# Performance work log

Measured on AMD Instinct MI355X. Metric: run time of the kernel, lower is better.

The kernel has to match this reference:

```python
import jax, jax.numpy as jnp
import numpy as np

B, S, D = 4, 2048, 1024
H, DK, DV = 16, 64, 64  # heads, key_size, size_per_head
NEG = 1000000000.0


def setup_inputs() -> dict:
    key = jax.random.key(0)
    ks = jax.random.split(key, 8)
    scale = 1.0 / np.sqrt(D)
    return {
        "q": jax.random.normal(ks[0], (B, S, D), jnp.float32),
        "k": jax.random.normal(ks[1], (B, S, D), jnp.float32),
        "v": jax.random.normal(ks[2], (B, S, D), jnp.float32),
        "v_mask": jax.random.randint(ks[3], (B, S), 0, 2).astype(jnp.float32),
        "q_mask": jax.random.randint(ks[4], (B, S), 0, 2).astype(jnp.float32),
        "Wq": jax.random.normal(ks[5], (D, H * DK), jnp.float32) * scale,
        "Wk": jax.random.normal(ks[6], (D, H * DK), jnp.float32) * scale,
        "Wv": jax.random.normal(ks[7], (D, H * DV), jnp.float32) * scale,
    }


def reference(q, k, v, v_mask, q_mask, Wq, Wk, Wv):
    b, sq, _ = q.shape
    sk = k.shape[1]
    # projections + head split: [B, H, S, Dh]
    qw = (q @ Wq).reshape(b, sq, H, DK).transpose(0, 2, 1, 3)
    kw = (k @ Wk).reshape(b, sk, H, DK).transpose(0, 2, 1, 3)
    vw = (v @ Wv).reshape(b, sk, H, DV).transpose(0, 2, 1, 3)
    # scaled dot-product scores [B, H, Sq, Sk]
    a = jnp.einsum("bhqd,bhkd->bhqk", qw, kw) / jnp.sqrt(jnp.float32(DK))
    # additive kv-mask (v_mask over key axis)
    a = a - (1.0 - v_mask)[:, None, None, :] * NEG
    # causal (mask_right=True): subtract 1e9 on strictly-upper triangle
    causal = jnp.triu(jnp.ones((sq, sk), jnp.float32), k=1) * NEG
    a = a - causal[None, None]
    a = jax.nn.softmax(a, axis=-1)
    o = jnp.einsum("bhqk,bhkd->bhqd", a, vw)
    o = o.transpose(0, 2, 1, 3).reshape(b, sq, H * DV)
    # multiplicative query mask on output
    return o * q_mask[:, :, None]
```

## Files before the change

kernel.cpp:

```cpp
#include <hip/hip_runtime.h>

#define S_LEN 2048
#define NHEAD 16

typedef float f32x4 __attribute__((ext_vector_type(4)));
typedef __bf16 bf16x8 __attribute__((ext_vector_type(8)));
typedef __bf16 bf16x4 __attribute__((ext_vector_type(4)));

#define AS1 __attribute__((address_space(1)))
#define AS3 __attribute__((address_space(3)))

__device__ __forceinline__ void gl2lds16(const void* g, void* l) {
    __builtin_amdgcn_global_load_lds((const AS1 unsigned int*)g,
                                     (AS3 unsigned int*)l, 16, 0, 0);
}
__device__ __forceinline__ void wb_leave4() {
    asm volatile("s_waitcnt vmcnt(4)\n\ts_barrier" ::: "memory");
}
__device__ __forceinline__ void wb_drain() {
    asm volatile("s_waitcnt vmcnt(0)\n\ts_barrier" ::: "memory");
}

__global__ __launch_bounds__(256) void cast_swizzle_kernel(
    const float* __restrict__ q, const float* __restrict__ k,
    const float* __restrict__ v, __bf16* __restrict__ out)
{
    int gid = blockIdx.x * 256 + threadIdx.x;
    int z   = gid >> 20;
    int rem = gid & 1048575;
    int r   = rem >> 7;
    int c   = rem & 127;
    const float* src = (z == 0 ? q : z == 1 ? k : v) + (size_t)r * 1024 + c * 8;
    float4 a = *(const float4*)src;
    float4 b = *(const float4*)(src + 4);
    bf16x8 t;
    t[0] = (__bf16)a.x; t[1] = (__bf16)a.y; t[2] = (__bf16)a.z; t[3] = (__bf16)a.w;
    t[4] = (__bf16)b.x; t[5] = (__bf16)b.y; t[6] = (__bf16)b.z; t[7] = (__bf16)b.w;
    int cp = (c & ~7) | ((c ^ r) & 7);
    *(bf16x8*)(out + (size_t)z * 8388608 + (size_t)r * 1024 + cp * 8) = t;
}

__global__ __launch_bounds__(256) void transpose_cast_kernel(
    const float* __restrict__ W0, const float* __restrict__ W1,
    const float* __restrict__ W2, __bf16* __restrict__ Wt)
{
    int z = blockIdx.z;
    const float* W = (z == 0 ? W0 : z == 1 ? W1 : W2);
    __bf16* out = Wt + (size_t)z * 1048576;
    __shared__ float tile[32][33];
    int bx = blockIdx.x, by = blockIdx.y;
    int tid = threadIdx.x;
    int tx = tid & 31, ty = tid >> 5;
    for (int i = 0; i < 32; i += 8)
        tile[ty + i][tx] = W[(size_t)(by * 32 + ty + i) * 1024 + bx * 32 + tx];
    __syncthreads();
    if (tid < 128) {
        int nl = tid >> 2, kc = tid & 3;
        int n = bx * 32 + nl;
        int kbase = by * 32 + kc * 8;
        bf16x8 t;
        for (int j = 0; j < 8; j++) t[j] = (__bf16)tile[kc * 8 + j][nl];
        int cp = ((kbase >> 3) ^ n) & 7;
        *(bf16x8*)(out + (size_t)n * 1024 + (kbase & ~63) + cp * 8) = t;
    }
}

__global__ __launch_bounds__(256, 3) void proj_gemm_kernel(
    const __bf16* __restrict__ Abf, const __bf16* __restrict__ Wt,
    __bf16* __restrict__ qw, __bf16* __restrict__ kw, __bf16* __restrict__ vt)
{
    int z = blockIdx.z;
    const __bf16* A = Abf + (size_t)z * 8388608;
    const __bf16* B = Wt + (size_t)z * 1048576;
    __shared__ __align__(16) char smem[49152];

    int tid = threadIdx.x;
    int bm = blockIdx.x, bn = blockIdx.y;
    int wave = tid >> 6, lane = tid & 63;
    int wm = (wave >> 1) * 64, wn = (wave & 1) * 64;
    int lrow = lane & 15;
    int q4 = lane >> 4;
    int l4r = lane >> 2, j4 = lane & 3;

    auto pf = [&](int kb) {
        int sl = kb % 3;
        int k0 = kb * 32;
        int segbyte = (k0 >> 6) * 128;
        int cbase = (k0 & 32) >> 3;
        for (int i = 0; i < 2; i++) {
            int r = wave * 32 + i * 16 + l4r;
            int cl = j4 ^ ((r >> 1) & 3);
            int phys = ((cbase + cl) ^ r) & 7;
            gl2lds16((const char*)A + (size_t)(bm * 128 + r) * 2048 + segbyte + phys * 16,
                     smem + sl * 8192 + wave * 2048 + i * 1024);
            gl2lds16((const char*)B + (size_t)(bn * 128 + r) * 2048 + segbyte + phys * 16,
                     smem + 24576 + sl * 8192 + wave * 2048 + i * 1024);
        }
    };

    f32x4 zero = {0.f, 0.f, 0.f, 0.f};
    f32x4 acc[4][4];
    for (int mt = 0; mt < 4; mt++)
        for (int nt = 0; nt < 4; nt++) acc[mt][nt] = zero;

    pf(0); pf(1);
    __syncthreads();
    for (int kb = 0; kb < 32; kb++) {
        if (kb == 31) wb_drain(); else wb_leave4();
        if (kb + 2 < 32) pf(kb + 2);
        int sA = (kb % 3) * 8192, sB = 24576 + (kb % 3) * 8192;
        bf16x8 af[4], bfv[4];
        for (int mt = 0; mt < 4; mt++) {
            int r = wm + mt * 16 + lrow;
            af[mt] = *(const bf16x8*)(smem + sA + r * 64 + (q4 ^ ((r >> 1) & 3)) * 16);
        }
        for (int nt = 0; nt < 4; nt++) {
            int r = wn + nt * 16 + lrow;
            bfv[nt] = *(const bf16x8*)(smem + sB + r * 64 + (q4 ^ ((r >> 1) & 3)) * 16);
        }
        for (int mt = 0; mt < 4; mt++)
            for (int nt = 0; nt < 4; nt++)
                acc[mt][nt] = __builtin_amdgcn_mfma_f32_16x16x32_bf16(
                    af[mt], bfv[nt], acc[mt][nt], 0, 0, 0);
    }
    __syncthreads();
    __bf16* T = (__bf16*)smem;

    float oscale = (z == 0) ? 0.125f : 1.0f;
    int rowoff = q4 * 4;
    int b = bm >> 4;
    int s_base = (bm & 15) * 128;
    if (z < 2) {
        for (int mt = 0; mt < 4; mt++) {
            for (int nt = 0; nt < 4; nt++) {
                int n_local = wn + nt * 16 + lrow;
                int hl = n_local >> 6, d = n_local & 63;
                for (int reg = 0; reg < 4; reg++) {
                    int s_local = wm + mt * 16 + rowoff + reg;
                    int s = s_base + s_local;
                    int dp = (d & 7) | ((((d >> 3) ^ s) & 7) << 3);
                    T[s_local * 136 + hl * 64 + dp] = (__bf16)(acc[mt][nt][reg] * oscale);
                }
            }
        }
        __syncthreads();
        char* gq = (char*)(z == 0 ? qw : kw);
        for (int i = 0; i < 8; i++) {
            int id = tid + i * 256;
            int hl = id >> 10, r = (id >> 3) & 127, j = id & 7;
            float4 val = *(float4*)((char*)T + r * 272 + hl * 128 + j * 16);
            *(float4*)(gq + ((size_t)((b * 16 + bn * 2 + hl) * 2048) + s_base + r) * 128
                          + j * 16) = val;
        }
    } else {
        for (int mt = 0; mt < 4; mt++) {
            int s0 = wm + mt * 16 + rowoff;
            int seg = s0 >> 6, j0 = s0 & 63;
            for (int nt = 0; nt < 4; nt++) {
                int n_local = wn + nt * 16 + lrow;
                int d = n_local & 63;
                int hi = ((j0 >> 3) ^ d) & 7;
                bf16x4 pk;
                for (int reg = 0; reg < 4; reg++) pk[reg] = (__bf16)acc[mt][nt][reg];
                *(bf16x4*)&T[n_local * 136 + seg * 64 + hi * 8 + (j0 & 7)] = pk;
            }
        }
        __syncthreads();
        char* gv = (char*)vt;
        for (int i = 0; i < 8; i++) {
            int id = tid + i * 256;
            int nl = id >> 4, j = id & 15;
            int hl = nl >> 6, dv = nl & 63;
            float4 val = *(float4*)((char*)T + nl * 272 + j * 16);
            *(float4*)(gv + (((size_t)((b * 16 + bn * 2 + hl) * 64 + dv)) * 2048 + s_base) * 2
                          + j * 16) = val;
        }
    }
}

__global__ __launch_bounds__(256, 2) void attn_kernel(
    const __bf16* __restrict__ QW, const __bf16* __restrict__ KW,
    const __bf16* __restrict__ VT, const float* __restrict__ v_mask,
    const float* __restrict__ q_mask, float* __restrict__ out)
{
    int lin = blockIdx.x + (blockIdx.y << 4);
    int xcd = lin & 7;
    int jj  = lin >> 3;
    int bh  = (xcd << 3) + (jj >> 4);
    int bx  = jj & 15;
    int b = bh >> 4, h = bh & 15;

    __shared__ __align__(16) char lds[34064];
    char*  Pw   = lds;
    float* lbuf = (float*)(lds + 32768);
    float* lfin = (float*)(lds + 33792);
    int*   flag = (int*)(lds + 34048);

    int tid = threadIdx.x;
    int wave = tid >> 6, lane = tid & 63;
    int mloc = lane & 15;
    int q4 = lane >> 4;
    int rowoff = q4 * 4;
    int x7 = mloc & 7;
    char* Pme = Pw + wave * 8192;

    const char* Krow = (const char*)KW + (size_t)bh * 2048 * 128;
    const char* Vrow = (const char*)VT + (size_t)bh * 64 * 4096;
    const float* vmrow = v_mask + (size_t)b * 2048;

    for (int p = 0; p < 2; p++) {
        int qb = p ? (31 - bx) : bx;
        const char* Qrow = (const char*)QW + ((size_t)bh * 2048 + qb * 64) * 128;

        if (tid == 0) *flag = 0;

        bf16x8 qfr[4][2];
        for (int nt = 0; nt < 4; nt++)
            for (int kc = 0; kc < 2; kc++)
                qfr[nt][kc] = *(const bf16x8*)(Qrow + (nt * 16 + mloc) * 128 +
                                               (((kc * 4 + q4) ^ x7) << 4));

        f32x4 zero = {0.f, 0.f, 0.f, 0.f};
        f32x4 o_acc[4][4];
        for (int mt = 0; mt < 4; mt++)
            for (int nt = 0; nt < 4; nt++) o_acc[mt][nt] = zero;
        float lt[4] = {0.f, 0.f, 0.f, 0.f};

        for (int kb = wave; kb <= qb; kb += 4) {
            bf16x8 vfr[4][2];
            for (int nt = 0; nt < 4; nt++)
                for (int kc = 0; kc < 2; kc++)
                    vfr[nt][kc] = *(const bf16x8*)(Vrow + (size_t)(nt * 16 + mloc) * 4096 +
                                                   kb * 128 + (((kc * 4 + q4) ^ x7) << 4));
            for (int half = 0; half < 2; half++) {
                bf16x8 kfr[2][2];
                for (int m2 = 0; m2 < 2; m2++)
                    for (int kc = 0; kc < 2; kc++)
                        kfr[m2][kc] = *(const bf16x8*)(Krow +
                            (size_t)(kb * 64 + (half * 2 + m2) * 16 + mloc) * 128 +
                            (((kc * 4 + q4) ^ x7) << 4));
                f32x4 sacc[2][4];
                for (int m2 = 0; m2 < 2; m2++)
                    for (int nt = 0; nt < 4; nt++) sacc[m2][nt] = zero;
                for (int kc = 0; kc < 2; kc++)
                    for (int m2 = 0; m2 < 2; m2++)
                        for (int nt = 0; nt < 4; nt++)
                            sacc[m2][nt] = __builtin_amdgcn_mfma_f32_16x16x32_bf16(
                                kfr[m2][kc], qfr[nt][kc], sacc[m2][nt], 0, 0, 0);
                for (int m2 = 0; m2 < 2; m2++) {
                    int mt = half * 2 + m2;
                    float4 vm4 = *(const float4*)(vmrow + kb * 64 + mt * 16 + rowoff);
                    float pen[4];
                    pen[0] = fmaf(1.0f - vm4.x, 1.0e9f, 12.0f);
                    pen[1] = fmaf(1.0f - vm4.y, 1.0e9f, 12.0f);
                    pen[2] = fmaf(1.0f - vm4.z, 1.0e9f, 12.0f);
                    pen[3] = fmaf(1.0f - vm4.w, 1.0e9f, 12.0f);
                    for (int nt = 0; nt < 4; nt++) {
                        float pv[4];
                        for (int reg = 0; reg < 4; reg++)
                            pv[reg] = __expf(sacc[m2][nt][reg] - pen[reg]);
                        if (kb == qb)
                            for (int reg = 0; reg < 4; reg++)
                                if (mt * 16 + rowoff + reg > nt * 16 + mloc) pv[reg] = 0.f;
                        lt[nt] += (pv[0] + pv[1]) + (pv[2] + pv[3]);
                        bf16x4 pk;
                        for (int reg = 0; reg < 4; reg++) pk[reg] = (__bf16)pv[reg];
                        *(bf16x4*)(Pme + (nt * 16 + mloc) * 128 +
                                   ((((mt * 2 + (q4 >> 1)) ^ x7)) << 4) + (q4 & 1) * 8) = pk;
                    }
                }
            }
            for (int mtq = 0; mtq < 4; mtq++)
                for (int kc = 0; kc < 2; kc++) {
                    bf16x8 afr = *(const bf16x8*)(Pme + (mtq * 16 + mloc) * 128 +
                                                  (((kc * 4 + q4) ^ x7) << 4));
                    for (int nt = 0; nt < 4; nt++)
                        o_acc[mtq][nt] = __builtin_amdgcn_mfma_f32_16x16x32_bf16(
                            afr, vfr[nt][kc], o_acc[mtq][nt], 0, 0, 0);
                }
        }

        for (int nt = 0; nt < 4; nt++) {
            lt[nt] += __shfl_xor(lt[nt], 16);
            lt[nt] += __shfl_xor(lt[nt], 32);
        }
        if (q4 == 0)
            for (int nt = 0; nt < 4; nt++)
                lbuf[(nt * 16 + mloc) * 4 + wave] = lt[nt];
        __syncthreads();
        float ltot[4];
        bool mydeg = false;
        for (int nt = 0; nt < 4; nt++) {
            float4 lv = *(const float4*)&lbuf[(nt * 16 + mloc) * 4];
            ltot[nt] = (lv.x + lv.y) + (lv.z + lv.w);
            mydeg |= (ltot[nt] == 0.0f);
        }
        if (mydeg && lane == 0) *flag = 1;
        __syncthreads();

        if (*flag) {
            float l2[4] = {0.f, 0.f, 0.f, 0.f};
            for (int kb = wave; kb < 32; kb += 4) {
                bf16x8 vfr[4][2];
                for (int nt = 0; nt < 4; nt++)
                    for (int kc = 0; kc < 2; kc++)
                        vfr[nt][kc] = *(const bf16x8*)(Vrow +
                            (size_t)(nt * 16 + mloc) * 4096 +
                            kb * 128 + (((kc * 4 + q4) ^ x7) << 4));
                for (int kc = 0; kc < 2; kc++) {
                    const float* vmp = vmrow + kb * 64 + kc * 32 + q4 * 8;
                    float4 va = *(const float4*)vmp;
                    float4 vb4 = *(const float4*)(vmp + 4);
                    float vmj[8] = {va.x, va.y, va.z, va.w, vb4.x, vb4.y, vb4.z, vb4.w};
                    int kg0 = kb * 64 + kc * 32 + q4 * 8;
                    for (int mtq = 0; mtq < 4; mtq++) {
                        bool degrow = (ltot[mtq] == 0.0f);
                        int qrow = qb * 64 + mtq * 16 + mloc;
                        bf16x8 af;
                        float cnt = 0.f;
                        for (int j = 0; j < 8; j++) {
                            float ind = degrow ? ((kg0 + j <= qrow) ? 1.0f : vmj[j]) : 0.0f;
                            af[j] = (__bf16)ind;
                            cnt += ind;
                        }
                        l2[mtq] += cnt;
                        for (int nt = 0; nt < 4; nt++)
                            o_acc[mtq][nt] = __builtin_amdgcn_mfma_f32_16x16x32_bf16(
                                af, vfr[nt][kc], o_acc[mtq][nt], 0, 0, 0);
                    }
                }
            }
            for (int mtq = 0; mtq < 4; mtq++) {
                l2[mtq] += __shfl_xor(l2[mtq], 16);
                l2[mtq] += __shfl_xor(l2[mtq], 32);
            }
            if (q4 == 0)
                for (int mtq = 0; mtq < 4; mtq++)
                    lbuf[(mtq * 16 + mloc) * 4 + wave] = l2[mtq];
            __syncthreads();
            for (int nt = 0; nt < 4; nt++) {
                if (ltot[nt] == 0.0f) {
                    float4 lv = *(const float4*)&lbuf[(nt * 16 + mloc) * 4];
                    ltot[nt] = (lv.x + lv.y) + (lv.z + lv.w);
                }
            }
        }

        if (wave == 0 && q4 == 0)
            for (int nt = 0; nt < 4; nt++)
                lfin[nt * 16 + mloc] = ltot[nt];

        for (int ch = 0; ch < 2; ch++) {
            float* Tme = (float*)Pme;
            for (int mtl = 0; mtl < 2; mtl++) {
                int mtq = ch * 2 + mtl;
                for (int nt = 0; nt < 4; nt++)
                    for (int reg = 0; reg < 4; reg++)
                        Tme[(mtl * 16 + rowoff + reg) * 64 + nt * 16 + mloc] =
                            o_acc[mtq][nt][reg];
            }
            __syncthreads();
            int q_rel = tid >> 3;
            int dv0 = (tid & 7) * 8;
            int qg = qb * 64 + ch * 32 + q_rel;
            float4 s0 = {0.f, 0.f, 0.f, 0.f}, s1 = {0.f, 0.f, 0.f, 0.f};
            for (int w = 0; w < 4; w++) {
                const float* base = (const float*)(Pw + w * 8192) + q_rel * 64 + dv0;
                float4 a = *(const float4*)base;
                float4 c = *(const float4*)(base + 4);
                s0.x += a.x; s0.y += a.y; s0.z += a.z; s0.w += a.w;
                s1.x += c.x; s1.y += c.y; s1.z += c.z; s1.w += c.w;
            }
            float scale = q_mask[b * 2048 + qg] / lfin[ch * 32 + q_rel];
            s0.x *= scale; s0.y *= scale; s0.z *= scale; s0.w *= scale;
            s1.x *= scale; s1.y *= scale; s1.z *= scale; s1.w *= scale;
            float* op = out + ((size_t)(b * 2048 + qg)) * 1024 + h * 64 + dv0;
            *(float4*)op = s0;
            *(float4*)(op + 4) = s1;
            __syncthreads();
        }
    }
}

extern "C" void kernel_launch(void* const* d_in, const int* in_sizes, int n_in,
                              void* d_out, int out_size, void* d_ws, size_t ws_size,
                              hipStream_t stream)
{
    const float* q      = (const float*)d_in[0];
    const float* k      = (const float*)d_in[1];
    const float* v      = (const float*)d_in[2];
    const float* v_mask = (const float*)d_in[3];
    const float* q_mask = (const float*)d_in[4];
    const float* Wq     = (const float*)d_in[5];
    const float* Wk     = (const float*)d_in[6];
    const float* Wv     = (const float*)d_in[7];
    float* out = (float*)d_out;

    __bf16* Abf = (__bf16*)d_ws;
    __bf16* Wt  = Abf + (size_t)3 * 8388608;
    __bf16* qw  = Wt + (size_t)3 * 1048576;
    __bf16* kw  = qw + (size_t)8388608;
    __bf16* vt  = kw + (size_t)8388608;

    cast_swizzle_kernel<<<12288, 256, 0, stream>>>(q, k, v, Abf);
    transpose_cast_kernel<<<dim3(32, 32, 3), 256, 0, stream>>>(Wq, Wk, Wv, Wt);
    proj_gemm_kernel<<<dim3(64, 8, 3), 256, 0, stream>>>(Abf, Wt, qw, kw, vt);
    attn_kernel<<<dim3(16, 64), 256, 0, stream>>>(qw, kw, vt, v_mask, q_mask, out);
}
```

Measured before the change: 314.1 us.

## Split attention work by query rows per wave with double-buffered K/V in LDS

The attention kernel changes from splitting key blocks across waves to giving each wave 16 query rows while all waves share each key block. K and V tiles are staged into LDS with async global-to-LDS loads and double-buffered, so the next block's load overlaps the current block's compute. The cross-wave reduction of partial outputs and row sums through LDS goes away, and each wave writes its output straight from registers. The cost is a block-wide barrier on every key block, less per-wave parallelism along the key axis, and more LDS, which may lower occupancy.

```diff
diff --git a/kernel.cpp b/kernel.cpp
--- a/kernel.cpp
+++ b/kernel.cpp
@@ -190,195 +190,157 @@
     int bx  = jj & 15;
     int b = bh >> 4, h = bh & 15;
 
-    __shared__ __align__(16) char lds[34064];
-    char*  Pw   = lds;
-    float* lbuf = (float*)(lds + 32768);
-    float* lfin = (float*)(lds + 33792);
-    int*   flag = (int*)(lds + 34048);
+    __shared__ __align__(16) char lds[40960];
+    char* Kb0 = lds;
+    char* Vb0 = lds + 16384;
+    char* Pw  = lds + 32768;
 
     int tid = threadIdx.x;
     int wave = tid >> 6, lane = tid & 63;
-    int mloc = lane & 15;
-    int q4 = lane >> 4;
-    int rowoff = q4 * 4;
-    int x7 = mloc & 7;
-    char* Pme = Pw + wave * 8192;
+    int mloc = lane & 15, q4 = lane >> 4;
+    int rowoff = q4 * 4, x7 = mloc & 7;
+    char* Pme = Pw + wave * 2048;
 
     const char* Krow = (const char*)KW + (size_t)bh * 2048 * 128;
     const char* Vrow = (const char*)VT + (size_t)bh * 64 * 4096;
     const float* vmrow = v_mask + (size_t)b * 2048;
 
+    int id0 = tid, id1 = tid + 256;
+
+    auto stage = [&](int kb, int slot) {
+        char* kd = Kb0 + slot * 8192;
+        char* vd = Vb0 + slot * 8192;
+        gl2lds16(Krow + (size_t)(kb * 64 + (id0 >> 3)) * 128 + (id0 & 7) * 16,
+                 kd + id0 * 16);
+        gl2lds16(Krow + (size_t)(kb * 64 + (id1 >> 3)) * 128 + (id1 & 7) * 16,
+                 kd + id1 * 16);
+        gl2lds16(Vrow + (size_t)(id0 >> 3) * 4096 + (size_t)kb * 128 + (id0 & 7) * 16,
+                 vd + id0 * 16);
+        gl2lds16(Vrow + (size_t)(id1 >> 3) * 4096 + (size_t)kb * 128 + (id1 & 7) * 16,
+                 vd + id1 * 16);
+    };
+
+    f32x4 zero = {0.f, 0.f, 0.f, 0.f};
+
     for (int p = 0; p < 2; p++) {
         int qb = p ? (31 - bx) : bx;
-        const char* Qrow = (const char*)QW + ((size_t)bh * 2048 + qb * 64) * 128;
-
-        if (tid == 0) *flag = 0;
-
-        bf16x8 qfr[4][2];
-        for (int nt = 0; nt < 4; nt++)
-            for (int kc = 0; kc < 2; kc++)
-                qfr[nt][kc] = *(const bf16x8*)(Qrow + (nt * 16 + mloc) * 128 +
+        const char* Qrow = (const char*)QW +
+                           ((size_t)bh * 2048 + qb * 64 + wave * 16) * 128;
+        bf16x8 qfr[2];
+        for (int kc = 0; kc < 2; kc++)
+            qfr[kc] = *(const bf16x8*)(Qrow + mloc * 128 + (((kc * 4 + q4) ^ x7) << 4));
+
+        stage(0, 0);
+
+        f32x4 o_acc[4];
+        for (int nt = 0; nt < 4; nt++) o_acc[nt] = zero;
+        float lt = 0.f;
+
+        for (int kb = 0; kb <= qb; kb++) {
+            int slot = kb & 1;
+            float4 vm4[4];
+            for (int m = 0; m < 4; m++)
+                vm4[m] = *(const float4*)(vmrow + kb * 64 + m * 16 + rowoff);
+            if (kb < qb) {
+                stage(kb + 1, slot ^ 1);
+                wb_leave4();
+            } else {
+                wb_drain();
+            }
+            const char* Kls = Kb0 + slot * 8192;
+            const char* Vls = Vb0 + slot * 8192;
+
+            f32x4 sacc[4];
+            for (int m = 0; m < 4; m++) sacc[m] = zero;
+            for (int kc = 0; kc < 2; kc++) {
+                bf16x8 kfr[4];
+                for (int m = 0; m < 4; m++)
+                    kfr[m] = *(const bf16x8*)(Kls + (m * 16 + mloc) * 128 +
+                                              (((kc * 4 + q4) ^ x7) << 4));
+                for (int m = 0; m < 4; m++)
+                    sacc[m] = __builtin_amdgcn_mfma_f32_16x16x32_bf16(
+                        kfr[m], qfr[kc], sacc[m], 0, 0, 0);
+            }
+            for (int m = 0; m < 4; m++) {
+                float pen[4];
+                pen[0] = fmaf(1.0f - vm4[m].x, 1.0e9f, 12.0f);
+                pen[1] = fmaf(1.0f - vm4[m].y, 1.0e9f, 12.0f);
+                pen[2] = fmaf(1.0f - vm4[m].z, 1.0e9f, 12.0f);
+                pen[3] = fmaf(1.0f - vm4[m].w, 1.0e9f, 12.0f);
+                float pv[4];
+                for (int reg = 0; reg < 4; reg++)
+                    pv[reg] = __expf(sacc[m][reg] - pen[reg]);
+                if (kb == qb)
+                    for (int reg = 0; reg < 4; reg++)
+                        if (m * 16 + rowoff + reg > wave * 16 + mloc) pv[reg] = 0.f;
+                lt += (pv[0] + pv[1]) + (pv[2] + pv[3]);
+                bf16x4 pk;
+                for (int reg = 0; reg < 4; reg++) pk[reg] = (__bf16)pv[reg];
+                *(bf16x4*)(Pme + mloc * 128 +
+                           (((m * 2 + (q4 >> 1)) ^ x7) << 4) + (q4 & 1) * 8) = pk;
+            }
+            for (int kc = 0; kc < 2; kc++) {
+                bf16x8 afr = *(const bf16x8*)(Pme + mloc * 128 +
+                                              (((kc * 4 + q4) ^ x7) << 4));
+                bf16x8 vfr[4];
+                for (int nt = 0; nt < 4; nt++)
+                    vfr[nt] = *(const bf16x8*)(Vls + (nt * 16 + mloc) * 128 +
                                                (((kc * 4 + q4) ^ x7) << 4));
-
-        f32x4 zero = {0.f, 0.f, 0.f, 0.f};
-        f32x4 o_acc[4][4];
-        for (int mt = 0; mt < 4; mt++)
-            for (int nt = 0; nt < 4; nt++) o_acc[mt][nt] = zero;
-        float lt[4] = {0.f, 0.f, 0.f, 0.f};
-
-        for (int kb = wave; kb <= qb; kb += 4) {
-            bf16x8 vfr[4][2];
-            for (int nt = 0; nt < 4; nt++)
-                for (int kc = 0; kc < 2; kc++)
-                    vfr[nt][kc] = *(const bf16x8*)(Vrow + (size_t)(nt * 16 + mloc) * 4096 +
-                                                   kb * 128 + (((kc * 4 + q4) ^ x7) << 4));
-            for (int half = 0; half < 2; half++) {
-                bf16x8 kfr[2][2];
-                for (int m2 = 0; m2 < 2; m2++)
-                    for (int kc = 0; kc < 2; kc++)
-                        kfr[m2][kc] = *(const bf16x8*)(Krow +
-                            (size_t)(kb * 64 + (half * 2 + m2) * 16 + mloc) * 128 +
-                            (((kc * 4 + q4) ^ x7) << 4));
-                f32x4 sacc[2][4];
-                for (int m2 = 0; m2 < 2; m2++)
-                    for (int nt = 0; nt < 4; nt++) sacc[m2][nt] = zero;
-                for (int kc = 0; kc < 2; kc++)
-                    for (int m2 = 0; m2 < 2; m2++)
-                        for (int nt = 0; nt < 4; nt++)
-                            sacc[m2][nt] = __builtin_amdgcn_mfma_f32_16x16x32_bf16(
-                                kfr[m2][kc], qfr[nt][kc], sacc[m2][nt], 0, 0, 0);
-                for (int m2 = 0; m2 < 2; m2++) {
-                    int mt = half * 2 + m2;
-                    float4 vm4 = *(const float4*)(vmrow + kb * 64 + mt * 16 + rowoff);
-                    float pen[4];
-                    pen[0] = fmaf(1.0f - vm4.x, 1.0e9f, 12.0f);
-                    pen[1] = fmaf(1.0f - vm4.y, 1.0e9f, 12.0f);
-                    pen[2] = fmaf(1.0f - vm4.z, 1.0e9f, 12.0f);
-                    pen[3] = fmaf(1.0f - vm4.w, 1.0e9f, 12.0f);
-                    for (int nt = 0; nt < 4; nt++) {
-                        float pv[4];
-                        for (int reg = 0; reg < 4; reg++)
-                            pv[reg] = __expf(sacc[m2][nt][reg] - pen[reg]);
-                        if (kb == qb)
-                            for (int reg = 0; reg < 4; reg++)
-                                if (mt * 16 + rowoff + reg > nt * 16 + mloc) pv[reg] = 0.f;
-                        lt[nt] += (pv[0] + pv[1]) + (pv[2] + pv[3]);
-                        bf16x4 pk;
-                        for (int reg = 0; reg < 4; reg++) pk[reg] = (__bf16)pv[reg];
-                        *(bf16x4*)(Pme + (nt * 16 + mloc) * 128 +
-                                   ((((mt * 2 + (q4 >> 1)) ^ x7)) << 4) + (q4 & 1) * 8) = pk;
-                    }
-                }
-            }
-            for (int mtq = 0; mtq < 4; mtq++)
-                for (int kc = 0; kc < 2; kc++) {
-                    bf16x8 afr = *(const bf16x8*)(Pme + (mtq * 16 + mloc) * 128 +
-                                                  (((kc * 4 + q4) ^ x7) << 4));
-                    for (int nt = 0; nt < 4; nt++)
-                        o_acc[mtq][nt] = __builtin_amdgcn_mfma_f32_16x16x32_bf16(
-                            afr, vfr[nt][kc], o_acc[mtq][nt], 0, 0, 0);
-                }
-        }
-
-        for (int nt = 0; nt < 4; nt++) {
-            lt[nt] += __shfl_xor(lt[nt], 16);
-            lt[nt] += __shfl_xor(lt[nt], 32);
-        }
-        if (q4 == 0)
-            for (int nt = 0; nt < 4; nt++)
-                lbuf[(nt * 16 + mloc) * 4 + wave] = lt[nt];
-        __syncthreads();
-        float ltot[4];
-        bool mydeg = false;
-        for (int nt = 0; nt < 4; nt++) {
-            float4 lv = *(const float4*)&lbuf[(nt * 16 + mloc) * 4];
-            ltot[nt] = (lv.x + lv.y) + (lv.z + lv.w);
-            mydeg |= (ltot[nt] == 0.0f);
-        }
-        if (mydeg && lane == 0) *flag = 1;
-        __syncthreads();
-
-        if (*flag) {
-            float l2[4] = {0.f, 0.f, 0.f, 0.f};
-            for (int kb = wave; kb < 32; kb += 4) {
+                for (int nt = 0; nt < 4; nt++)
+                    o_acc[nt] = __builtin_amdgcn_mfma_f32_16x16x32_bf16(
+                        afr, vfr[nt], o_acc[nt], 0, 0, 0);
+            }
+            __syncthreads();
+        }
+
+        lt += __shfl_xor(lt, 16);
+        lt += __shfl_xor(lt, 32);
+
+        if (__any(lt == 0.0f)) {
+            float l2 = 0.f;
+            bool degrow = (lt == 0.0f);
+            int qrow = qb * 64 + wave * 16 + mloc;
+            for (int kb2 = 0; kb2 < 32; kb2++) {
                 bf16x8 vfr[4][2];
                 for (int nt = 0; nt < 4; nt++)
                     for (int kc = 0; kc < 2; kc++)
                         vfr[nt][kc] = *(const bf16x8*)(Vrow +
                             (size_t)(nt * 16 + mloc) * 4096 +
-                            kb * 128 + (((kc * 4 + q4) ^ x7) << 4));
+                            kb2 * 128 + (((kc * 4 + q4) ^ x7) << 4));
                 for (int kc = 0; kc < 2; kc++) {
-                    const float* vmp = vmrow + kb * 64 + kc * 32 + q4 * 8;
+                    const float* vmp = vmrow + kb2 * 64 + kc * 32 + q4 * 8;
                     float4 va = *(const float4*)vmp;
                     float4 vb4 = *(const float4*)(vmp + 4);
-                    float vmj[8] = {va.x, va.y, va.z, va.w, vb4.x, vb4.y, vb4.z, vb4.w};
-                    int kg0 = kb * 64 + kc * 32 + q4 * 8;
-                    for (int mtq = 0; mtq < 4; mtq++) {
-                        bool degrow = (ltot[mtq] == 0.0f);
-                        int qrow = qb * 64 + mtq * 16 + mloc;
-                        bf16x8 af;
-                        float cnt = 0.f;
-                        for (int j = 0; j < 8; j++) {
-                            float ind = degrow ? ((kg0 + j <= qrow) ? 1.0f : vmj[j]) : 0.0f;
-                            af[j] = (__bf16)ind;
-                            cnt += ind;
-                        }
-                        l2[mtq] += cnt;
-                        for (int nt = 0; nt < 4; nt++)
-                            o_acc[mtq][nt] = __builtin_amdgcn_mfma_f32_16x16x32_bf16(
-                                af, vfr[nt][kc], o_acc[mtq][nt], 0, 0, 0);
+                    float vmj[8] = {va.x, va.y, va.z, va.w,
+                                    vb4.x, vb4.y, vb4.z, vb4.w};
+                    int kg0 = kb2 * 64 + kc * 32 + q4 * 8;
+                    bf16x8 af;
+                    float cnt = 0.f;
+                    for (int j = 0; j < 8; j++) {
+                        float ind = degrow ? ((kg0 + j <= qrow) ? 1.0f : vmj[j]) : 0.0f;
+                        af[j] = (__bf16)ind;
+                        cnt += ind;
                     }
+                    l2 += cnt;
+                    for (int nt = 0; nt < 4; nt++)
+                        o_acc[nt] = __builtin_amdgcn_mfma_f32_16x16x32_bf16(
+                            af, vfr[nt][kc], o_acc[nt], 0, 0, 0);
                 }
             }
-            for (int mtq = 0; mtq < 4; mtq++) {
-                l2[mtq] += __shfl_xor(l2[mtq], 16);
-                l2[mtq] += __shfl_xor(l2[mtq], 32);
-            }
-            if (q4 == 0)
-                for (int mtq = 0; mtq < 4; mtq++)
-                    lbuf[(mtq * 16 + mloc) * 4 + wave] = l2[mtq];
-            __syncthreads();
-            for (int nt = 0; nt < 4; nt++) {
-                if (ltot[nt] == 0.0f) {
-                    float4 lv = *(const float4*)&lbuf[(nt * 16 + mloc) * 4];
-                    ltot[nt] = (lv.x + lv.y) + (lv.z + lv.w);
-                }
-            }
-        }
-
-        if (wave == 0 && q4 == 0)
-            for (int nt = 0; nt < 4; nt++)
-                lfin[nt * 16 + mloc] = ltot[nt];
-
-        for (int ch = 0; ch < 2; ch++) {
-            float* Tme = (float*)Pme;
-            for (int mtl = 0; mtl < 2; mtl++) {
-                int mtq = ch * 2 + mtl;
-                for (int nt = 0; nt < 4; nt++)
-                    for (int reg = 0; reg < 4; reg++)
-                        Tme[(mtl * 16 + rowoff + reg) * 64 + nt * 16 + mloc] =
-                            o_acc[mtq][nt][reg];
-            }
-            __syncthreads();
-            int q_rel = tid >> 3;
-            int dv0 = (tid & 7) * 8;
-            int qg = qb * 64 + ch * 32 + q_rel;
-            float4 s0 = {0.f, 0.f, 0.f, 0.f}, s1 = {0.f, 0.f, 0.f, 0.f};
-            for (int w = 0; w < 4; w++) {
-                const float* base = (const float*)(Pw + w * 8192) + q_rel * 64 + dv0;
-                float4 a = *(const float4*)base;
-                float4 c = *(const float4*)(base + 4);
-                s0.x += a.x; s0.y += a.y; s0.z += a.z; s0.w += a.w;
-                s1.x += c.x; s1.y += c.y; s1.z += c.z; s1.w += c.w;
-            }
-            float scale = q_mask[b * 2048 + qg] / lfin[ch * 32 + q_rel];
-            s0.x *= scale; s0.y *= scale; s0.z *= scale; s0.w *= scale;
-            s1.x *= scale; s1.y *= scale; s1.z *= scale; s1.w *= scale;
-            float* op = out + ((size_t)(b * 2048 + qg)) * 1024 + h * 64 + dv0;
-            *(float4*)op = s0;
-            *(float4*)(op + 4) = s1;
-            __syncthreads();
-        }
+            l2 += __shfl_xor(l2, 16);
+            l2 += __shfl_xor(l2, 32);
+            if (degrow) lt = l2;
+        }
+
+        float sc[4];
+        for (int reg = 0; reg < 4; reg++) {
+            float lq = __shfl(lt, rowoff + reg);
+            sc[reg] = q_mask[b * 2048 + qb * 64 + wave * 16 + rowoff + reg] / lq;
+        }
+        for (int nt = 0; nt < 4; nt++)
+            for (int reg = 0; reg < 4; reg++)
+                out[((size_t)(b * 2048 + qb * 64 + wave * 16 + rowoff + reg)) * 1024 +
+                    h * 64 + nt * 16 + mloc] = o_acc[nt][reg] * sc[reg];
     }
 }
 
```

New measurement: 308.2 us. Within noise of the previous version (-1.9%).
